# Kernel optimization log

Measured on AMD Instinct MI355X. Metric: run time of the kernel, lower is better.

Reference implementation:

```python
import jax, jax.numpy as jnp
import numpy as np

B, T, E, H = 4, 4096, 1024, 64

def setup_inputs() -> dict:
    key = jax.random.key(0)
    k1, k2, k3, k4 = jax.random.split(key, 4)
    x = jax.random.normal(k1, (B, T, E), dtype=jnp.float32)
    # nn.Linear(E, H, bias=False): weight [H, E]; store as [E, H] for x @ W
    scale = 1.0 / np.sqrt(E)
    Wk = jax.random.normal(k2, (E, H), dtype=jnp.float32) * scale
    Wq = jax.random.normal(k3, (E, H), dtype=jnp.float32) * scale
    Wv = jax.random.normal(k4, (E, H), dtype=jnp.float32) * scale
    return {"x": x, "Wk": Wk, "Wq": Wq, "Wv": Wv}

def reference(x, Wk, Wq, Wv):
    Bc, Tc, Ec = x.shape
    k = x @ Wk            # [B, T, H]
    q = x @ Wq            # [B, T, H]
    v = x @ Wv            # [B, T, H]
    # NOTE: original scales by 1/sqrt(embedding_size), not head_size
    scores = jnp.einsum('bqh,bkh->bqk', q, k) / jnp.sqrt(jnp.float32(Ec))
    causal = jnp.tril(jnp.ones((Tc, Tc), dtype=bool))
    scores = jnp.where(causal, scores, -jnp.inf)
    weights = jax.nn.softmax(scores, axis=-1)
    return jnp.einsum('bqk,bkh->bqh', weights, v)
```

## Files before the change

kernel.cpp:

```cpp
#include <hip/hip_runtime.h>

#define B_ 4
#define T_ 4096
#define E_ 1024
#define H_ 64

typedef __attribute__((ext_vector_type(8))) short short8;
typedef __attribute__((ext_vector_type(4))) float f32x4;

static __device__ __forceinline__ unsigned short f2bf(float f) {
    unsigned int u = __builtin_bit_cast(unsigned int, f);
    u += 0x7fffu + ((u >> 16) & 1u);
    return (unsigned short)(u >> 16);
}
static __device__ __forceinline__ float bf2f(unsigned short h) {
    unsigned int u = ((unsigned int)h) << 16;
    return __builtin_bit_cast(float, u);
}
#if __has_builtin(__builtin_amdgcn_exp2f)
#define EXP2(x) __builtin_amdgcn_exp2f(x)
#else
#define EXP2(x) exp2f(x)
#endif

#define GLOBAL_AS __attribute__((address_space(1)))
#define LDS_AS    __attribute__((address_space(3)))

__global__ __launch_bounds__(256) void wt_transpose_kernel(
    const float* __restrict__ Wq, const float* __restrict__ Wk,
    const float* __restrict__ Wv, unsigned short* __restrict__ Wt)
{
    __shared__ float tile[64][65];
    const int mat = blockIdx.x >> 4;
    const int kt  = blockIdx.x & 15;
    const float* W = (mat == 0) ? Wq : ((mat == 1) ? Wk : Wv);
    const int tid = threadIdx.x;
    #pragma unroll
    for (int p = 0; p < 16; ++p) {
        int idx = p * 256 + tid;
        tile[idx >> 6][idx & 63] = W[(kt * 64 + (idx >> 6)) * 64 + (idx & 63)];
    }
    __syncthreads();
    #pragma unroll
    for (int p = 0; p < 16; ++p) {
        int idx = p * 256 + tid;
        int h = idx >> 6, kl = idx & 63;
        Wt[(mat * 64 + h) * E_ + kt * 64 + kl] = f2bf(tile[kl][h]);
    }
}

__global__ __launch_bounds__(256) void proj_kernel(
    const float* __restrict__ x, const unsigned short* __restrict__ Wt,
    unsigned short* __restrict__ Qb, unsigned short* __restrict__ Kb,
    unsigned short* __restrict__ Vt)
{
    __shared__ unsigned short wt_lds[192][72];
    const int tid  = threadIdx.x;
    const int wid  = tid >> 6, lane = tid & 63;
    const int g    = lane >> 4, c = lane & 15;
    const int r0   = blockIdx.x * 64;
    const float QSCALE = 0.03125f * 1.44269504088896f;

    f32x4 acc[3][4];
    #pragma unroll
    for (int m = 0; m < 3; ++m)
        #pragma unroll
        for (int n = 0; n < 4; ++n) acc[m][n] = 0.0f;

    const float* xrow = x + (size_t)(r0 + wid * 16 + c) * E_;

    for (int kk = 0; kk < E_; kk += 64) {
        #pragma unroll
        for (int p = 0; p < 6; ++p) {
            int cidx = p * 256 + tid;
            int kchunk = cidx & 7;
            int hrow = cidx >> 3;
            *(short8*)&wt_lds[hrow][kchunk * 8] =
                *(const short8*)&Wt[hrow * E_ + kk + kchunk * 8];
        }
        __syncthreads();
        #pragma unroll
        for (int kc = 0; kc < 2; ++kc) {
            f32x4 xa = *(const f32x4*)&xrow[kk + kc * 32 + 8 * g];
            f32x4 xb = *(const f32x4*)&xrow[kk + kc * 32 + 8 * g + 4];
            short8 a;
            #pragma unroll
            for (int j = 0; j < 4; ++j) {
                a[j]     = (short)f2bf(xa[j]);
                a[j + 4] = (short)f2bf(xb[j]);
            }
            #pragma unroll
            for (int m = 0; m < 3; ++m)
                #pragma unroll
                for (int n = 0; n < 4; ++n) {
                    short8 b = *(const short8*)&wt_lds[m * 64 + n * 16 + c][kc * 32 + 8 * g];
                    acc[m][n] = __builtin_amdgcn_mfma_f32_16x16x32_bf16(a, b, acc[m][n], 0, 0, 0);
                }
        }
        __syncthreads();
    }

    const int bb = r0 >> 12;
    #pragma unroll
    for (int n = 0; n < 4; ++n)
        #pragma unroll
        for (int r = 0; r < 4; ++r) {
            int row = r0 + wid * 16 + 4 * g + r;
            int col = n * 16 + c;
            Qb[(size_t)row * H_ + col] = f2bf(acc[0][n][r] * QSCALE);
            Kb[(size_t)row * H_ + col] = f2bf(acc[1][n][r]);
            Vt[((size_t)bb * H_ + col) * T_ + (row & (T_ - 1))] = f2bf(acc[2][n][r]);
        }
}

__global__ __launch_bounds__(256, 3) void attn_split_kernel(
    const unsigned short* __restrict__ Qb, const unsigned short* __restrict__ Kb,
    const unsigned short* __restrict__ Vt, unsigned short* __restrict__ Po,
    float* __restrict__ Pl)
{
    __shared__ unsigned short K_lds[2][64][64];
    __shared__ unsigned short V_lds[2][64][64];
    __shared__ unsigned short p_lds[4][16][72];
    const int tid   = threadIdx.x;
    const int wid   = tid >> 6, lane = tid & 63;
    const int g     = lane >> 4, c = lane & 15;

    const int s     = blockIdx.x * 4 + wid;
    const int batch = s >> 11;
    const int rem   = s & 2047;
    const int ch    = rem >> 8;
    const int qt    = rem & 255;
    const int nkv   = (qt >> 2) + 1;
    if (ch * 8 >= nkv) return;
    const int nt    = min(8, nkv - ch * 8);
    const int qbase = qt * 16;
    const int lastt = nkv - 1 - ch * 8;

    const int Mm = nkv - 1, aa = Mm >> 3, rr8 = Mm & 7;
    const int npart = (nkv + 7) >> 3;
    const int slot  = batch * 1152 + 4 * (4 * aa * (aa + 1) + rr8 * (aa + 1))
                    + (qt & 3) * npart + ch;

    const int rsub = lane >> 3;
    const int csw  = (lane & 7) ^ rsub;
    const int cs0 = (g ^ (c & 7)) * 8;
    const int cs1 = ((g + 4) ^ (c & 7)) * 8;

    short8 aq0, aq1;
    {
        const unsigned short* qp = Qb + ((size_t)(batch * T_ + qbase + c)) * H_ + 8 * g;
        aq0 = *(const short8*)&qp[0];
        aq1 = *(const short8*)&qp[32];
    }

    short8 ones;
    #pragma unroll
    for (int j = 0; j < 8; ++j) ones[j] = (short)0x3F80;

    f32x4 o_acc[4];
    #pragma unroll
    for (int n = 0; n < 4; ++n) o_acc[n] = 0.0f;
    f32x4 l_acc = 0.0f;

    auto stage = [&](int buf, int gt) {
        const int key0 = gt * 64;
        #pragma unroll
        for (int j = 0; j < 2; ++j) {
            const int row = wid * 16 + j * 8;
            const unsigned short* gk = Kb
                + ((size_t)(batch * T_ + key0 + row + rsub)) * H_ + csw * 8;
            __builtin_amdgcn_global_load_lds(
                (const GLOBAL_AS unsigned int*)gk,
                (LDS_AS unsigned int*)&K_lds[buf][row][0], 16, 0, 0);
            const unsigned short* gv = Vt
                + ((size_t)(batch * H_ + row + rsub)) * T_ + key0 + csw * 8;
            __builtin_amdgcn_global_load_lds(
                (const GLOBAL_AS unsigned int*)gv,
                (LDS_AS unsigned int*)&V_lds[buf][row][0], 16, 0, 0);
        }
    };

    stage(0, ch * 8);
    __syncthreads();

    for (int t = 0; t < nt; ++t) {
        const int buf = t & 1;
        if (t + 1 < nt) stage(buf ^ 1, ch * 8 + t + 1);

        f32x4 sA[4];
        #pragma unroll
        for (int n = 0; n < 4; ++n) sA[n] = 0.0f;
        #pragma unroll
        for (int n = 0; n < 4; ++n) {
            short8 bk0 = *(const short8*)&K_lds[buf][n * 16 + c][cs0];
            short8 bk1 = *(const short8*)&K_lds[buf][n * 16 + c][cs1];
            sA[n] = __builtin_amdgcn_mfma_f32_16x16x32_bf16(aq0, bk0, sA[n], 0, 0, 0);
            sA[n] = __builtin_amdgcn_mfma_f32_16x16x32_bf16(aq1, bk1, sA[n], 0, 0, 0);
        }

        float pv[4][4];
        #pragma unroll
        for (int n = 0; n < 4; ++n)
            #pragma unroll
            for (int r = 0; r < 4; ++r)
                pv[n][r] = EXP2(sA[n][r]);
        if (t == lastt) {
            const int d = (ch * 8 + t) * 64 + c - qbase - 4 * g;
            #pragma unroll
            for (int n = 0; n < 4; ++n)
                #pragma unroll
                for (int r = 0; r < 4; ++r)
                    if (d + 16 * n > r) pv[n][r] = 0.0f;
        }

        #pragma unroll
        for (int n = 0; n < 4; ++n)
            #pragma unroll
            for (int r = 0; r < 4; ++r)
                p_lds[wid][4 * g + r][n * 16 + c] = f2bf(pv[n][r]);
        short8 pa0 = *(const short8*)&p_lds[wid][c][8 * g];
        short8 pa1 = *(const short8*)&p_lds[wid][c][32 + 8 * g];

        l_acc = __builtin_amdgcn_mfma_f32_16x16x32_bf16(pa0, ones, l_acc, 0, 0, 0);
        l_acc = __builtin_amdgcn_mfma_f32_16x16x32_bf16(pa1, ones, l_acc, 0, 0, 0);

        #pragma unroll
        for (int n = 0; n < 4; ++n) {
            short8 bv0 = *(const short8*)&V_lds[buf][n * 16 + c][cs0];
            short8 bv1 = *(const short8*)&V_lds[buf][n * 16 + c][cs1];
            o_acc[n] = __builtin_amdgcn_mfma_f32_16x16x32_bf16(pa0, bv0, o_acc[n], 0, 0, 0);
            o_acc[n] = __builtin_amdgcn_mfma_f32_16x16x32_bf16(pa1, bv1, o_acc[n], 0, 0, 0);
        }

        __syncthreads();
    }

    unsigned short* po = Po + (size_t)slot * 1024;
    #pragma unroll
    for (int n = 0; n < 4; ++n)
        #pragma unroll
        for (int r = 0; r < 4; ++r)
            po[(4 * g + r) * 64 + n * 16 + c] = f2bf(o_acc[n][r]);
    if (c == 0) {
        #pragma unroll
        for (int r = 0; r < 4; ++r)
            Pl[slot * 16 + 4 * g + r] = l_acc[r];
    }
}

__global__ __launch_bounds__(256) void attn_merge_kernel(
    const unsigned short* __restrict__ Po, const float* __restrict__ Pl,
    float* __restrict__ out)
{
    const int tid  = threadIdx.x;
    const int wid  = tid >> 6, lane = tid & 63;
    const int gi   = blockIdx.x * 4 + wid;
    const int batch = gi >> 8, qt = gi & 255;
    const int nkv  = (qt >> 2) + 1;
    const int npart = (nkv + 7) >> 3;
    const int Mm = nkv - 1, aa = Mm >> 3, rr8 = Mm & 7;
    const int slot0 = batch * 1152 + 4 * (4 * aa * (aa + 1) + rr8 * (aa + 1))
                    + (qt & 3) * npart;

    const int row = lane & 15, seg = lane >> 4;

    float lacc = 0.0f, o[16];
    #pragma unroll
    for (int k = 0; k < 16; ++k) o[k] = 0.0f;

    for (int i = 0; i < npart; ++i) {
        lacc += Pl[(slot0 + i) * 16 + row];
        const unsigned short* pp = Po + (size_t)(slot0 + i) * 1024 + row * 64 + seg * 16;
        short8 v0 = *(const short8*)&pp[0];
        short8 v1 = *(const short8*)&pp[8];
        #pragma unroll
        for (int k = 0; k < 8; ++k) {
            o[k]     += bf2f((unsigned short)v0[k]);
            o[8 + k] += bf2f((unsigned short)v1[k]);
        }
    }

    const float inv = 1.0f / lacc;
    float* op = out + ((size_t)(batch * T_ + qt * 16 + row)) * H_ + seg * 16;
    #pragma unroll
    for (int k = 0; k < 16; ++k) op[k] = o[k] * inv;
}

extern "C" void kernel_launch(void* const* d_in, const int* in_sizes, int n_in,
                              void* d_out, int out_size, void* d_ws, size_t ws_size,
                              hipStream_t stream)
{
    const float* x  = (const float*)d_in[0];
    const float* Wk = (const float*)d_in[1];
    const float* Wq = (const float*)d_in[2];
    const float* Wv = (const float*)d_in[3];
    float* out = (float*)d_out;

    unsigned short* Wt = (unsigned short*)d_ws;
    unsigned short* Qb = Wt + 3 * 64 * 1024;
    unsigned short* Kb = Qb + (size_t)B_ * T_ * H_;
    unsigned short* Vt = Kb + (size_t)B_ * T_ * H_;
    unsigned short* Po = Vt + (size_t)B_ * T_ * H_;
    float* Pl = (float*)(Po + (size_t)4608 * 1024);

    hipLaunchKernelGGL(wt_transpose_kernel, dim3(48), dim3(256), 0, stream, Wq, Wk, Wv, Wt);
    hipLaunchKernelGGL(proj_kernel, dim3(256), dim3(256), 0, stream, x, Wt, Qb, Kb, Vt);
    hipLaunchKernelGGL(attn_split_kernel, dim3(2048), dim3(256), 0, stream, Qb, Kb, Vt, Po, Pl);
    hipLaunchKernelGGL(attn_merge_kernel, dim3(256), dim3(256), 0, stream, Po, Pl, out);
}
```

Baseline: 72.94 us.

## Double-buffer projection tiles via global_load_lds with 768-thread blocks split by matrix

Measured after the change: 67.94 us. 6.9% less time.

```diff
diff --git a/kernel.cpp b/kernel.cpp
--- a/kernel.cpp
+++ b/kernel.cpp
@@ -49,40 +49,68 @@
     }
 }
 
-__global__ __launch_bounds__(256) void proj_kernel(
+__global__ __launch_bounds__(768, 1) void proj_kernel(
     const float* __restrict__ x, const unsigned short* __restrict__ Wt,
     unsigned short* __restrict__ Qb, unsigned short* __restrict__ Kb,
     unsigned short* __restrict__ Vt)
 {
-    __shared__ unsigned short wt_lds[192][72];
+    __shared__ float          x_lds[2][4096];
+    __shared__ unsigned short wt_lds[2][12288];
     const int tid  = threadIdx.x;
     const int wid  = tid >> 6, lane = tid & 63;
     const int g    = lane >> 4, c = lane & 15;
+    const int mat  = wid >> 2;
+    const int rg   = wid & 3;
     const int r0   = blockIdx.x * 64;
     const float QSCALE = 0.03125f * 1.44269504088896f;
 
-    f32x4 acc[3][4];
-    #pragma unroll
-    for (int m = 0; m < 3; ++m)
-        #pragma unroll
-        for (int n = 0; n < 4; ++n) acc[m][n] = 0.0f;
-
-    const float* xrow = x + (size_t)(r0 + wid * 16 + c) * E_;
-
-    for (int kk = 0; kk < E_; kk += 64) {
-        #pragma unroll
-        for (int p = 0; p < 6; ++p) {
-            int cidx = p * 256 + tid;
-            int kchunk = cidx & 7;
-            int hrow = cidx >> 3;
-            *(short8*)&wt_lds[hrow][kchunk * 8] =
-                *(const short8*)&Wt[hrow * E_ + kk + kchunk * 8];
-        }
-        __syncthreads();
+    auto stage = [&](int buf, int kk) {
+        {
+            int row = tid >> 4, ch = tid & 15;
+            int csw = ch ^ (row & 15);
+            const float* src = x + (size_t)(r0 + row) * E_ + kk + csw * 4;
+            __builtin_amdgcn_global_load_lds(
+                (const GLOBAL_AS unsigned int*)src,
+                (LDS_AS unsigned int*)&x_lds[buf][(tid & ~63) * 4], 16, 0, 0);
+            if (tid < 256) {
+                int idx2 = 768 + tid;
+                int row2 = idx2 >> 4, ch2 = idx2 & 15;
+                int csw2 = ch2 ^ (row2 & 15);
+                const float* src2 = x + (size_t)(r0 + row2) * E_ + kk + csw2 * 4;
+                __builtin_amdgcn_global_load_lds(
+                    (const GLOBAL_AS unsigned int*)src2,
+                    (LDS_AS unsigned int*)&x_lds[buf][(idx2 & ~63) * 4], 16, 0, 0);
+            }
+        }
+        #pragma unroll
+        for (int p = 0; p < 2; ++p) {
+            int idx = p * 768 + tid;
+            int row = idx >> 3, ch = idx & 7;
+            int csw = ch ^ (row & 7);
+            const unsigned short* src = Wt + (size_t)row * E_ + kk + csw * 8;
+            __builtin_amdgcn_global_load_lds(
+                (const GLOBAL_AS unsigned int*)src,
+                (LDS_AS unsigned int*)&wt_lds[buf][(idx & ~63) * 8], 16, 0, 0);
+        }
+    };
+
+    f32x4 acc[4];
+    #pragma unroll
+    for (int n = 0; n < 4; ++n) acc[n] = 0.0f;
+
+    stage(0, 0);
+    __syncthreads();
+
+    for (int t = 0; t < 16; ++t) {
+        const int buf = t & 1;
+        if (t < 15) stage(buf ^ 1, (t + 1) * 64);
+
+        const int xrowbase = (rg * 16 + c) * 64;
+        const int wrowbase = (mat * 64 + c) * 64;
         #pragma unroll
         for (int kc = 0; kc < 2; ++kc) {
-            f32x4 xa = *(const f32x4*)&xrow[kk + kc * 32 + 8 * g];
-            f32x4 xb = *(const f32x4*)&xrow[kk + kc * 32 + 8 * g + 4];
+            f32x4 xa = *(const f32x4*)&x_lds[buf][xrowbase + ((8 * kc + 2 * g)     ^ c) * 4];
+            f32x4 xb = *(const f32x4*)&x_lds[buf][xrowbase + ((8 * kc + 2 * g + 1) ^ c) * 4];
             short8 a;
             #pragma unroll
             for (int j = 0; j < 4; ++j) {
@@ -90,12 +118,11 @@
                 a[j + 4] = (short)f2bf(xb[j]);
             }
             #pragma unroll
-            for (int m = 0; m < 3; ++m)
-                #pragma unroll
-                for (int n = 0; n < 4; ++n) {
-                    short8 b = *(const short8*)&wt_lds[m * 64 + n * 16 + c][kc * 32 + 8 * g];
-                    acc[m][n] = __builtin_amdgcn_mfma_f32_16x16x32_bf16(a, b, acc[m][n], 0, 0, 0);
-                }
+            for (int n = 0; n < 4; ++n) {
+                short8 b = *(const short8*)
+                    &wt_lds[buf][wrowbase + n * 1024 + (((4 * kc + g) ^ (c & 7)) * 8)];
+                acc[n] = __builtin_amdgcn_mfma_f32_16x16x32_bf16(a, b, acc[n], 0, 0, 0);
+            }
         }
         __syncthreads();
     }
@@ -105,11 +132,15 @@
     for (int n = 0; n < 4; ++n)
         #pragma unroll
         for (int r = 0; r < 4; ++r) {
-            int row = r0 + wid * 16 + 4 * g + r;
+            int row = r0 + rg * 16 + 4 * g + r;
             int col = n * 16 + c;
-            Qb[(size_t)row * H_ + col] = f2bf(acc[0][n][r] * QSCALE);
-            Kb[(size_t)row * H_ + col] = f2bf(acc[1][n][r]);
-            Vt[((size_t)bb * H_ + col) * T_ + (row & (T_ - 1))] = f2bf(acc[2][n][r]);
+            float v = acc[n][r];
+            if (mat == 0)
+                Qb[(size_t)row * H_ + col] = f2bf(v * QSCALE);
+            else if (mat == 1)
+                Kb[(size_t)row * H_ + col] = f2bf(v);
+            else
+                Vt[((size_t)bb * H_ + col) * T_ + (row & (T_ - 1))] = f2bf(v);
         }
 }
 
@@ -304,7 +335,7 @@
     float* Pl = (float*)(Po + (size_t)4608 * 1024);
 
     hipLaunchKernelGGL(wt_transpose_kernel, dim3(48), dim3(256), 0, stream, Wq, Wk, Wv, Wt);
-    hipLaunchKernelGGL(proj_kernel, dim3(256), dim3(256), 0, stream, x, Wt, Qb, Kb, Vt);
+    hipLaunchKernelGGL(proj_kernel, dim3(256), dim3(768), 0, stream, x, Wt, Qb, Kb, Vt);
     hipLaunchKernelGGL(attn_split_kernel, dim3(2048), dim3(256), 0, stream, Qb, Kb, Vt, Po, Pl);
     hipLaunchKernelGGL(attn_merge_kernel, dim3(256), dim3(256), 0, stream, Po, Pl, out);
 }
```
